# Performance work log

Measured on AMD Instinct MI355X. Metric: run time of the kernel, lower is better.

The kernel has to match this reference:

```python
import jax, jax.numpy as jnp
import numpy as np

LN_EPS = 1e-5


def setup_inputs() -> dict:
    key = jax.random.key(0)
    ks = jax.random.split(key, 6)
    B, M, N, D = 16, 128, 128, 128
    NM, H = 16, 512
    xav = float(np.sqrt(2.0 / (D + D)))  # xavier_normal over (in_dim, out_dim) fan
    return {
        "x": jax.random.normal(ks[0], (B, M, N, D), jnp.float32),
        "w1": jax.random.normal(ks[1], (D, D, NM, 2), jnp.float32) * xav,
        "w2": jax.random.normal(ks[2], (D, D, NM, 2), jnp.float32) * xav,
        "ff_w0": jax.random.normal(ks[3], (D, H), jnp.float32) * float(1.0 / np.sqrt(D)),
        "ff_b0": jnp.zeros((H,), jnp.float32),
        "ff_w1": jax.random.normal(ks[4], (H, D), jnp.float32) * float(1.0 / np.sqrt(H)),
        "ff_b1": jnp.zeros((D,), jnp.float32),
        "ln_g": jnp.ones((D,), jnp.float32),
        "ln_b": jnp.zeros((D,), jnp.float32),
    }


def _layer_norm(h, g, b):
    mu = jnp.mean(h, axis=-1, keepdims=True)
    var = jnp.mean(jnp.square(h - mu), axis=-1, keepdims=True)
    return (h - mu) * jax.lax.rsqrt(var + LN_EPS) * g + b


def _forward_fourier(x, w1, w2):
    # x: [B, M, N, I] -> [B, I, M, N]
    xt = jnp.transpose(x, (0, 3, 1, 2))
    B, I, M, N = xt.shape
    nm = w1.shape[2]
    cw1 = w1[..., 0] + 1j * w1[..., 1]  # [I, O, nm]
    cw2 = w2[..., 0] + 1j * w2[..., 1]
    O = cw1.shape[1]

    # Fourier along last axis (y)
    fty = jnp.fft.rfft(xt, axis=-1, norm="ortho")                    # [B,I,M,N//2+1]
    f1 = jnp.einsum("bixy,ioy->boxy", fty[..., :nm], cw1)            # [B,O,M,nm]
    pad_y = jnp.zeros((B, O, M, N // 2 + 1 - nm), dtype=f1.dtype)
    xy = jnp.fft.irfft(jnp.concatenate([f1, pad_y], axis=-1), n=N, axis=-1, norm="ortho")

    # Fourier along second-to-last axis (x)
    ftx = jnp.fft.rfft(xt, axis=-2, norm="ortho")                    # [B,I,M//2+1,N]
    f2 = jnp.einsum("bixy,iox->boxy", ftx[:, :, :nm, :], cw2)        # [B,O,nm,N]
    pad_x = jnp.zeros((B, O, M // 2 + 1 - nm, N), dtype=f2.dtype)
    xx = jnp.fft.irfft(jnp.concatenate([f2, pad_x], axis=-2), n=M, axis=-2, norm="ortho")

    return jnp.transpose(xx + xy, (0, 2, 3, 1))  # [B,M,N,O]


def reference(x, w1, w2, ff_w0, ff_b0, ff_w1, ff_b1, ln_g, ln_b):
    h = _forward_fourier(x, w1, w2)
    # backcast FeedForward: Linear -> ReLU -> Linear -> LayerNorm (dropout=0)
    h1 = jax.nn.relu(jnp.einsum("bmni,ih->bmnh", h, ff_w0) + ff_b0)
    h2 = jnp.einsum("bmnh,ho->bmno", h1, ff_w1) + ff_b1
    return _layer_norm(h2, ln_g, ln_b)
```

## Files before the change

kernel.cpp:

```cpp
#include <hip/hip_runtime.h>


#define LN_EPS 1e-5f
#define NMODES 16
#define FROW 4096
#define HROW 16384

typedef __attribute__((ext_vector_type(8))) short short8;
typedef __attribute__((ext_vector_type(4))) float f32x4;

__device__ __forceinline__ ushort f2bf(float f) {
    unsigned u = __float_as_uint(f);
    unsigned r = (u + 0x7FFFu + ((u >> 16) & 1u)) >> 16;
    return (ushort)r;
}

__global__ void k_setup(float* __restrict__ Tc, float* __restrict__ Ts,
                        float* __restrict__ IT) {
    const float invs = 0.08838834764831845f;
    for (int idx = threadIdx.x; idx < NMODES * 128; idx += blockDim.x) {
        int k = idx >> 7, n = idx & 127;
        int p = (k * n) & 127;
        float th = (float)p * (6.283185307179586f / 128.0f);
        float c = cosf(th), s = sinf(th);
        Tc[idx] = c * invs;
        Ts[idx] = -s * invs;
        float ck = (k == 0) ? invs : 2.0f * invs;
        IT[n * 32 + 2 * k]     = ck * c;
        IT[n * 32 + 2 * k + 1] = -ck * s;
    }
}

__global__ void k_wpack(const float* __restrict__ w, float* __restrict__ Wp) {
    int idx = blockIdx.x * 256 + threadIdx.x;
    int k  = idx >> 16;
    int ip = (idx >> 8) & 255;
    int op = idx & 255;
    int i = ip & 127, o = op & 127;
    const float* base = w + (((i << 7) | o) * NMODES + k) * 2;
    float re = base[0], im = base[1];
    float v = (ip < 128) ? ((op < 128) ? re : im)
                         : ((op < 128) ? -im : re);
    Wp[idx] = v;
}

__global__ __launch_bounds__(256) void k_wcvt(const float* __restrict__ w0,
        const float* __restrict__ w1, ushort* __restrict__ w0t,
        ushort* __restrict__ w1t) {
    int idx = blockIdx.x * 256 + threadIdx.x;
    int h = idx >> 7, k = idx & 127;
    w0t[idx] = f2bf(w0[k * 512 + h]);
    int o = idx >> 9, hh = idx & 511;
    w1t[idx] = f2bf(w1[hh * 128 + o]);
}

__global__ __launch_bounds__(128) void k_fft(const float* __restrict__ x,
        const float* __restrict__ Tc, const float* __restrict__ Ts,
        float* __restrict__ F, int mode) {
    __shared__ float Tc_s[NMODES * 128];
    __shared__ float Ts_s[NMODES * 128];
    for (int e = threadIdx.x; e < NMODES * 128; e += 128) {
        Tc_s[e] = Tc[e];
        Ts_s[e] = Ts[e];
    }
    __syncthreads();
    int row = blockIdx.x;
    int base, ts;
    if (mode == 0) { base = row * HROW; ts = 128; }
    else { base = (row >> 7) * 2097152 + (row & 127) * 128; ts = 16384; }
    int i = threadIdx.x;
    float re[NMODES], im[NMODES];
#pragma unroll
    for (int k = 0; k < NMODES; ++k) { re[k] = 0.f; im[k] = 0.f; }
    for (int tb = 0; tb < 32; ++tb) {
        int t0 = tb * 4;
        float xv0 = x[base + (t0 + 0) * ts + i];
        float xv1 = x[base + (t0 + 1) * ts + i];
        float xv2 = x[base + (t0 + 2) * ts + i];
        float xv3 = x[base + (t0 + 3) * ts + i];
#pragma unroll
        for (int k = 0; k < NMODES; ++k) {
            f32x4 c4 = *(const f32x4*)&Tc_s[k * 128 + t0];
            f32x4 s4 = *(const f32x4*)&Ts_s[k * 128 + t0];
            re[k] += xv0 * c4[0] + xv1 * c4[1] + xv2 * c4[2] + xv3 * c4[3];
            im[k] += xv0 * s4[0] + xv1 * s4[1] + xv2 * s4[2] + xv3 * s4[3];
        }
    }
    float* outp = F + row * FROW;
#pragma unroll
    for (int k = 0; k < NMODES; ++k) {
        outp[k * 256 + i]       = re[k];
        outp[k * 256 + 128 + i] = im[k];
    }
}

__global__ __launch_bounds__(256) void k_mix(const float* __restrict__ A,
        const float* __restrict__ Wp, float* __restrict__ outF) {
    __shared__ float A_s[256 * 36];
    int kt = blockIdx.x & 15;
    int bm0 = (blockIdx.x >> 4) * 32;
    for (int e = threadIdx.x; e < 32 * 256; e += 256) {
        int r = e >> 8, c = e & 255;
        A_s[c * 36 + r] = A[(bm0 + r) * FROW + kt * 256 + c];
    }
    __syncthreads();
    int tc = threadIdx.x & 63, tr = threadIdx.x >> 6;
    float acc[8][4];
#pragma unroll
    for (int j = 0; j < 8; ++j)
#pragma unroll
        for (int q = 0; q < 4; ++q) acc[j][q] = 0.f;
    const float* wp = Wp + kt * 65536 + tc * 4;
    for (int kk = 0; kk < 256; ++kk) {
        f32x4 wv = *(const f32x4*)(wp + kk * 256);
        f32x4 a0 = *(const f32x4*)&A_s[kk * 36 + tr * 8];
        f32x4 a1 = *(const f32x4*)&A_s[kk * 36 + tr * 8 + 4];
#pragma unroll
        for (int q = 0; q < 4; ++q) {
            acc[0][q] += a0[0] * wv[q]; acc[1][q] += a0[1] * wv[q];
            acc[2][q] += a0[2] * wv[q]; acc[3][q] += a0[3] * wv[q];
            acc[4][q] += a1[0] * wv[q]; acc[5][q] += a1[1] * wv[q];
            acc[6][q] += a1[2] * wv[q]; acc[7][q] += a1[3] * wv[q];
        }
    }
#pragma unroll
    for (int j = 0; j < 8; ++j) {
        f32x4 v = { acc[j][0], acc[j][1], acc[j][2], acc[j][3] };
        *(f32x4*)&outF[(bm0 + tr * 8 + j) * FROW + kt * 256 + tc * 4] = v;
    }
}

__global__ __launch_bounds__(256) void k_icdft(const float* __restrict__ f,
        const float* __restrict__ IT, float* __restrict__ h, int mode) {
    __shared__ float IT_s[128 * 32];
    __shared__ float f_s[32 * 128];
    int row = blockIdx.x;
    for (int e = threadIdx.x; e < 4096; e += 256) {
        IT_s[e] = IT[e];
        f_s[e]  = f[row * FROW + e];
    }
    __syncthreads();
    int o = threadIdx.x & 127, nh = threadIdx.x >> 7;
    int outbase, ostride;
    if (mode == 0) { outbase = row * HROW + o; ostride = 128; }
    else { outbase = (row >> 7) * 2097152 + (row & 127) * 128 + o; ostride = 16384; }
    for (int nb = 0; nb < 8; ++nb) {
        int n0 = nh * 64 + nb * 8;
        float acc[8];
#pragma unroll
        for (int j = 0; j < 8; ++j) acc[j] = 0.f;
#pragma unroll
        for (int kpb = 0; kpb < 8; ++kpb) {
            int kp0 = kpb * 4;
            float f0 = f_s[kp0 * 128 + o];
            float f1v = f_s[kp0 * 128 + 128 + o];
            float f2v = f_s[kp0 * 128 + 256 + o];
            float f3v = f_s[kp0 * 128 + 384 + o];
#pragma unroll
            for (int j = 0; j < 8; ++j) {
                f32x4 it = *(const f32x4*)&IT_s[(n0 + j) * 32 + kp0];
                acc[j] += f0 * it[0] + f1v * it[1] + f2v * it[2] + f3v * it[3];
            }
        }
        if (mode == 0) {
#pragma unroll
            for (int j = 0; j < 8; ++j) h[outbase + (n0 + j) * ostride] = acc[j];
        } else {
#pragma unroll
            for (int j = 0; j < 8; ++j) h[outbase + (n0 + j) * ostride] += acc[j];
        }
    }
}

__global__ __launch_bounds__(256) void k_ffn(float* __restrict__ hio,
        const ushort* __restrict__ w0t, const float* __restrict__ b0,
        const ushort* __restrict__ w1t, const float* __restrict__ b1,
        const float* __restrict__ g, const float* __restrict__ bb) {
    __shared__ __align__(16) char smem[33792 + 1024 + 512];
    ushort* h1_s = (ushort*)smem;
    float*  h2_s = (float*)smem;
    float*  gb_s = (float*)(smem + 33792);
    float*  mr_s = (float*)(smem + 34816);

    int tid = threadIdx.x;
    int R0 = blockIdx.x * 64;
    if (tid < 128) { gb_s[tid] = g[tid]; gb_s[128 + tid] = bb[tid]; }

    int lane = tid & 63, wid = tid >> 6;
    int frow = lane & 15;
    int fk8 = (lane >> 4) * 8;
    int fr4 = (lane >> 4) * 4;

    short8 a1f[4][4];
#pragma unroll
    for (int tr = 0; tr < 4; ++tr)
#pragma unroll
        for (int kk = 0; kk < 4; ++kk) {
            const float* src = &hio[(R0 + tr * 16 + frow) * 128 + kk * 32 + fk8];
            f32x4 v0 = *(const f32x4*)src;
            f32x4 v1 = *(const f32x4*)(src + 4);
            short8 t;
#pragma unroll
            for (int j = 0; j < 4; ++j) {
                t[j]     = (short)f2bf(v0[j]);
                t[4 + j] = (short)f2bf(v1[j]);
            }
            a1f[tr][kk] = t;
        }

    f32x4 acc2[4][2];
#pragma unroll
    for (int a = 0; a < 4; ++a)
#pragma unroll
        for (int c = 0; c < 2; ++c) acc2[a][c] = {0.f, 0.f, 0.f, 0.f};

    for (int hc = 0; hc < 2; ++hc) {
        __syncthreads();
#pragma unroll
        for (int tc = 0; tc < 4; ++tc) {
            int hcol = hc * 256 + wid * 64 + tc * 16 + frow;
            short8 bfr[4];
#pragma unroll
            for (int kk = 0; kk < 4; ++kk)
                bfr[kk] = *(const short8*)&w0t[hcol * 128 + kk * 32 + fk8];
            f32x4 acc1[4];
#pragma unroll
            for (int a = 0; a < 4; ++a) acc1[a] = {0.f, 0.f, 0.f, 0.f};
#pragma unroll
            for (int kk = 0; kk < 4; ++kk)
#pragma unroll
                for (int tr = 0; tr < 4; ++tr)
                    acc1[tr] = __builtin_amdgcn_mfma_f32_16x16x32_bf16(
                        a1f[tr][kk], bfr[kk], acc1[tr], 0, 0, 0);
            float b0v = b0[hcol];
            int lcol = wid * 64 + tc * 16 + frow;
#pragma unroll
            for (int tr = 0; tr < 4; ++tr)
#pragma unroll
                for (int r = 0; r < 4; ++r) {
                    float v = acc1[tr][r] + b0v;
                    h1_s[(tr * 16 + fr4 + r) * 264 + lcol] = f2bf(fmaxf(v, 0.f));
                }
        }
        __syncthreads();
#pragma unroll
        for (int kk = 0; kk < 8; ++kk) {
            short8 a2[4];
#pragma unroll
            for (int tr = 0; tr < 4; ++tr)
                a2[tr] = *(const short8*)&h1_s[(tr * 16 + frow) * 264 + kk * 32 + fk8];
#pragma unroll
            for (int tc = 0; tc < 2; ++tc) {
                int ocol = wid * 32 + tc * 16 + frow;
                short8 b2 = *(const short8*)&w1t[ocol * 512 + hc * 256 + kk * 32 + fk8];
#pragma unroll
                for (int tr = 0; tr < 4; ++tr)
                    acc2[tr][tc] = __builtin_amdgcn_mfma_f32_16x16x32_bf16(
                        a2[tr], b2, acc2[tr][tc], 0, 0, 0);
            }
        }
    }
    __syncthreads();
#pragma unroll
    for (int tc = 0; tc < 2; ++tc) {
        int ocol = wid * 32 + tc * 16 + frow;
        float b1v = b1[ocol];
#pragma unroll
        for (int tr = 0; tr < 4; ++tr)
#pragma unroll
            for (int r = 0; r < 4; ++r)
                h2_s[(tr * 16 + fr4 + r) * 132 + ocol] = acc2[tr][tc][r] + b1v;
    }
    __syncthreads();
    int row = tid >> 2, sub = tid & 3;
    const float* hr = &h2_s[row * 132 + sub * 32];
    float s = 0.f;
#pragma unroll
    for (int j = 0; j < 32; ++j) s += hr[j];
    s += __shfl_xor(s, 1); s += __shfl_xor(s, 2);
    float mu = s * (1.0f / 128.0f);
    float s2 = 0.f;
#pragma unroll
    for (int j = 0; j < 32; ++j) { float dv = hr[j] - mu; s2 += dv * dv; }
    s2 += __shfl_xor(s2, 1); s2 += __shfl_xor(s2, 2);
    float rstd = rsqrtf(s2 * (1.0f / 128.0f) + LN_EPS);
    if (sub == 0) { mr_s[row * 2] = mu; mr_s[row * 2 + 1] = rstd; }
    __syncthreads();
    for (int e = tid; e < 2048; e += 256) {
        int r = e >> 5, d4 = (e & 31) * 4;
        float mu2 = mr_s[r * 2], rs = mr_s[r * 2 + 1];
        f32x4 v = *(const f32x4*)&h2_s[r * 132 + d4];
        f32x4 o;
#pragma unroll
        for (int j = 0; j < 4; ++j)
            o[j] = (v[j] - mu2) * rs * gb_s[d4 + j] + gb_s[128 + d4 + j];
        *(f32x4*)&hio[(R0 + r) * 128 + d4] = o;
    }
}

extern "C" void kernel_launch(void* const* d_in, const int* in_sizes, int n_in,
                              void* d_out, int out_size, void* d_ws, size_t ws_size,
                              hipStream_t stream) {
    (void)in_sizes; (void)n_in; (void)out_size; (void)ws_size;
    const float* x   = (const float*)d_in[0];
    const float* w1  = (const float*)d_in[1];
    const float* w2  = (const float*)d_in[2];
    const float* fw0 = (const float*)d_in[3];
    const float* fb0 = (const float*)d_in[4];
    const float* fw1 = (const float*)d_in[5];
    const float* fb1 = (const float*)d_in[6];
    const float* lng = (const float*)d_in[7];
    const float* lnb = (const float*)d_in[8];
    float* out = (float*)d_out;

    char* ws = (char*)d_ws;
    float* Tc   = (float*)(ws);
    float* Ts   = (float*)(ws + 8192);
    float* IT   = (float*)(ws + 16384);
    float* Wp   = (float*)(ws + 32768);
    float* buf0 = (float*)(ws + 32768 + 4194304);
    float* buf1 = (float*)(ws + 32768 + 4194304 + 33554432);

    k_setup<<<1, 256, 0, stream>>>(Tc, Ts, IT);

    k_wpack<<<4096, 256, 0, stream>>>(w1, Wp);
    k_fft  <<<2048, 128, 0, stream>>>(x, Tc, Ts, buf0, 0);
    k_mix  <<<1024, 256, 0, stream>>>(buf0, Wp, buf1);
    k_icdft<<<2048, 256, 0, stream>>>(buf1, IT, out, 0);

    k_wpack<<<4096, 256, 0, stream>>>(w2, Wp);
    k_fft  <<<2048, 128, 0, stream>>>(x, Tc, Ts, buf0, 1);
    k_mix  <<<1024, 256, 0, stream>>>(buf0, Wp, buf1);

    ushort* w0t = (ushort*)buf0;
    ushort* w1t = (ushort*)(buf0 + 65536);
    k_wcvt <<<256, 256, 0, stream>>>(fw0, fw1, w0t, w1t);

    k_icdft<<<2048, 256, 0, stream>>>(buf1, IT, out, 1);

    k_ffn<<<4096, 256, 0, stream>>>(out, w0t, fb0, w1t, fb1, lng, lnb);
}
```

Measured before the change: 585.2 us.

## Move spectral mixing onto bf16x3 MFMA and fuse LayerNorm into FFN registers

The fp32 FMA spectral mixing GEMM is replaced by an MFMA version that splits operands into bf16 hi/lo pairs and uses three products to keep near-fp32 accuracy. Weights are packed transposed into hi/lo bf16 buffers. The FFN kernel now processes the hidden dimension in four chunks with a smaller shared-memory tile, caches biases in LDS, and computes LayerNorm statistics directly from accumulators via shuffles using a one-pass sum/sum-of-squares, avoiding the h2 staging round trip. Risks include slight precision loss from the split-bf16 scheme and the single-pass variance formula.

```diff
diff --git a/kernel.cpp b/kernel.cpp
--- a/kernel.cpp
+++ b/kernel.cpp
@@ -7,12 +7,16 @@
 #define HROW 16384
 
 typedef __attribute__((ext_vector_type(8))) short short8;
+typedef __attribute__((ext_vector_type(4))) short short4v;
 typedef __attribute__((ext_vector_type(4))) float f32x4;
 
 __device__ __forceinline__ ushort f2bf(float f) {
     unsigned u = __float_as_uint(f);
     unsigned r = (u + 0x7FFFu + ((u >> 16) & 1u)) >> 16;
     return (ushort)r;
+}
+__device__ __forceinline__ float bf2f(ushort h) {
+    return __uint_as_float(((unsigned)h) << 16);
 }
 
 __global__ void k_setup(float* __restrict__ Tc, float* __restrict__ Ts,
@@ -31,17 +35,21 @@
     }
 }
 
-__global__ void k_wpack(const float* __restrict__ w, float* __restrict__ Wp) {
+__global__ void k_wpack(const float* __restrict__ w, ushort* __restrict__ Wph,
+                        ushort* __restrict__ Wpl) {
     int idx = blockIdx.x * 256 + threadIdx.x;
     int k  = idx >> 16;
-    int ip = (idx >> 8) & 255;
-    int op = idx & 255;
+    int op = (idx >> 8) & 255;
+    int ip = idx & 255;
     int i = ip & 127, o = op & 127;
     const float* base = w + (((i << 7) | o) * NMODES + k) * 2;
     float re = base[0], im = base[1];
     float v = (ip < 128) ? ((op < 128) ? re : im)
                          : ((op < 128) ? -im : re);
-    Wp[idx] = v;
+    ushort hi = f2bf(v);
+    ushort lo = f2bf(v - bf2f(hi));
+    Wph[idx] = hi;
+    Wpl[idx] = lo;
 }
 
 __global__ __launch_bounds__(256) void k_wcvt(const float* __restrict__ w0,
@@ -94,40 +102,71 @@
     }
 }
 
-__global__ __launch_bounds__(256) void k_mix(const float* __restrict__ A,
-        const float* __restrict__ Wp, float* __restrict__ outF) {
-    __shared__ float A_s[256 * 36];
+__global__ __launch_bounds__(256) void k_mixm(const float* __restrict__ A,
+        const ushort* __restrict__ Wph, const ushort* __restrict__ Wpl,
+        float* __restrict__ outF) {
+    __shared__ ushort Ah[32 * 264];
+    __shared__ ushort Al[32 * 264];
+    int tid = threadIdx.x;
     int kt = blockIdx.x & 15;
     int bm0 = (blockIdx.x >> 4) * 32;
-    for (int e = threadIdx.x; e < 32 * 256; e += 256) {
-        int r = e >> 8, c = e & 255;
-        A_s[c * 36 + r] = A[(bm0 + r) * FROW + kt * 256 + c];
-    }
-    __syncthreads();
-    int tc = threadIdx.x & 63, tr = threadIdx.x >> 6;
-    float acc[8][4];
-#pragma unroll
-    for (int j = 0; j < 8; ++j)
-#pragma unroll
-        for (int q = 0; q < 4; ++q) acc[j][q] = 0.f;
-    const float* wp = Wp + kt * 65536 + tc * 4;
-    for (int kk = 0; kk < 256; ++kk) {
-        f32x4 wv = *(const f32x4*)(wp + kk * 256);
-        f32x4 a0 = *(const f32x4*)&A_s[kk * 36 + tr * 8];
-        f32x4 a1 = *(const f32x4*)&A_s[kk * 36 + tr * 8 + 4];
-#pragma unroll
-        for (int q = 0; q < 4; ++q) {
-            acc[0][q] += a0[0] * wv[q]; acc[1][q] += a0[1] * wv[q];
-            acc[2][q] += a0[2] * wv[q]; acc[3][q] += a0[3] * wv[q];
-            acc[4][q] += a1[0] * wv[q]; acc[5][q] += a1[1] * wv[q];
-            acc[6][q] += a1[2] * wv[q]; acc[7][q] += a1[3] * wv[q];
-        }
-    }
-#pragma unroll
-    for (int j = 0; j < 8; ++j) {
-        f32x4 v = { acc[j][0], acc[j][1], acc[j][2], acc[j][3] };
-        *(f32x4*)&outF[(bm0 + tr * 8 + j) * FROW + kt * 256 + tc * 4] = v;
-    }
+    {
+        int row = tid >> 3, cg = tid & 7;
+        const float* arow = A + (bm0 + row) * FROW + kt * 256 + cg * 32;
+        ushort* ah = &Ah[row * 264 + cg * 32];
+        ushort* al = &Al[row * 264 + cg * 32];
+#pragma unroll
+        for (int j = 0; j < 8; ++j) {
+            f32x4 v = *(const f32x4*)(arow + j * 4);
+            short4v h4, l4;
+#pragma unroll
+            for (int q = 0; q < 4; ++q) {
+                ushort h = f2bf(v[q]);
+                h4[q] = (short)h;
+                l4[q] = (short)f2bf(v[q] - bf2f(h));
+            }
+            *(short4v*)(ah + j * 4) = h4;
+            *(short4v*)(al + j * 4) = l4;
+        }
+    }
+    __syncthreads();
+    int lane = tid & 63, wid = tid >> 6;
+    int frow = lane & 15, fk8 = (lane >> 4) * 8, fr4 = (lane >> 4) * 4;
+    f32x4 acc[2][4];
+#pragma unroll
+    for (int a = 0; a < 2; ++a)
+#pragma unroll
+        for (int c = 0; c < 4; ++c) acc[a][c] = {0.f, 0.f, 0.f, 0.f};
+    const ushort* wph = Wph + kt * 65536;
+    const ushort* wpl = Wpl + kt * 65536;
+#pragma unroll
+    for (int kk = 0; kk < 8; ++kk) {
+        short8 ah0 = *(const short8*)&Ah[(frow)      * 264 + kk * 32 + fk8];
+        short8 ah1 = *(const short8*)&Ah[(16 + frow) * 264 + kk * 32 + fk8];
+        short8 al0 = *(const short8*)&Al[(frow)      * 264 + kk * 32 + fk8];
+        short8 al1 = *(const short8*)&Al[(16 + frow) * 264 + kk * 32 + fk8];
+#pragma unroll
+        for (int tc = 0; tc < 4; ++tc) {
+            int op = wid * 64 + tc * 16 + frow;
+            int base = op * 256 + kk * 32 + fk8;
+            short8 wh = *(const short8*)&wph[base];
+            short8 wl = *(const short8*)&wpl[base];
+            acc[0][tc] = __builtin_amdgcn_mfma_f32_16x16x32_bf16(ah0, wh, acc[0][tc], 0, 0, 0);
+            acc[0][tc] = __builtin_amdgcn_mfma_f32_16x16x32_bf16(ah0, wl, acc[0][tc], 0, 0, 0);
+            acc[0][tc] = __builtin_amdgcn_mfma_f32_16x16x32_bf16(al0, wh, acc[0][tc], 0, 0, 0);
+            acc[1][tc] = __builtin_amdgcn_mfma_f32_16x16x32_bf16(ah1, wh, acc[1][tc], 0, 0, 0);
+            acc[1][tc] = __builtin_amdgcn_mfma_f32_16x16x32_bf16(ah1, wl, acc[1][tc], 0, 0, 0);
+            acc[1][tc] = __builtin_amdgcn_mfma_f32_16x16x32_bf16(al1, wh, acc[1][tc], 0, 0, 0);
+        }
+    }
+#pragma unroll
+    for (int tr = 0; tr < 2; ++tr)
+#pragma unroll
+        for (int tc = 0; tc < 4; ++tc)
+#pragma unroll
+            for (int r = 0; r < 4; ++r)
+                outF[(bm0 + tr * 16 + fr4 + r) * FROW + kt * 256 + wid * 64 + tc * 16 + frow]
+                    = acc[tr][tc][r];
 }
 
 __global__ __launch_bounds__(256) void k_icdft(const float* __restrict__ f,
@@ -176,15 +215,22 @@
         const ushort* __restrict__ w0t, const float* __restrict__ b0,
         const ushort* __restrict__ w1t, const float* __restrict__ b1,
         const float* __restrict__ g, const float* __restrict__ bb) {
-    __shared__ __align__(16) char smem[33792 + 1024 + 512];
-    ushort* h1_s = (ushort*)smem;
-    float*  h2_s = (float*)smem;
-    float*  gb_s = (float*)(smem + 33792);
-    float*  mr_s = (float*)(smem + 34816);
+    __shared__ __align__(16) ushort h1_s[64 * 136];
+    __shared__ float b0_s[512];
+    __shared__ float gb_s[256];
+    __shared__ float b1_s[128];
+    __shared__ float ps_s[64 * 4];
+    __shared__ float pq_s[64 * 4];
+    __shared__ float mr_s[64 * 2];
 
     int tid = threadIdx.x;
     int R0 = blockIdx.x * 64;
-    if (tid < 128) { gb_s[tid] = g[tid]; gb_s[128 + tid] = bb[tid]; }
+    for (int e = tid; e < 512; e += 256) b0_s[e] = b0[e];
+    if (tid < 128) {
+        gb_s[tid] = g[tid];
+        gb_s[128 + tid] = bb[tid];
+        b1_s[tid] = b1[tid];
+    }
 
     int lane = tid & 63, wid = tid >> 6;
     int frow = lane & 15;
@@ -214,11 +260,12 @@
 #pragma unroll
         for (int c = 0; c < 2; ++c) acc2[a][c] = {0.f, 0.f, 0.f, 0.f};
 
-    for (int hc = 0; hc < 2; ++hc) {
+    for (int hc = 0; hc < 4; ++hc) {
         __syncthreads();
 #pragma unroll
-        for (int tc = 0; tc < 4; ++tc) {
-            int hcol = hc * 256 + wid * 64 + tc * 16 + frow;
+        for (int tc = 0; tc < 2; ++tc) {
+            int lcol = wid * 32 + tc * 16 + frow;
+            int hcol = hc * 128 + lcol;
             short8 bfr[4];
 #pragma unroll
             for (int kk = 0; kk < 4; ++kk)
@@ -232,27 +279,26 @@
                 for (int tr = 0; tr < 4; ++tr)
                     acc1[tr] = __builtin_amdgcn_mfma_f32_16x16x32_bf16(
                         a1f[tr][kk], bfr[kk], acc1[tr], 0, 0, 0);
-            float b0v = b0[hcol];
-            int lcol = wid * 64 + tc * 16 + frow;
+            float b0v = b0_s[hcol];
 #pragma unroll
             for (int tr = 0; tr < 4; ++tr)
 #pragma unroll
                 for (int r = 0; r < 4; ++r) {
                     float v = acc1[tr][r] + b0v;
-                    h1_s[(tr * 16 + fr4 + r) * 264 + lcol] = f2bf(fmaxf(v, 0.f));
+                    h1_s[(tr * 16 + fr4 + r) * 136 + lcol] = f2bf(fmaxf(v, 0.f));
                 }
         }
         __syncthreads();
 #pragma unroll
-        for (int kk = 0; kk < 8; ++kk) {
+        for (int kk = 0; kk < 4; ++kk) {
             short8 a2[4];
 #pragma unroll
             for (int tr = 0; tr < 4; ++tr)
-                a2[tr] = *(const short8*)&h1_s[(tr * 16 + frow) * 264 + kk * 32 + fk8];
+                a2[tr] = *(const short8*)&h1_s[(tr * 16 + frow) * 136 + kk * 32 + fk8];
 #pragma unroll
             for (int tc = 0; tc < 2; ++tc) {
                 int ocol = wid * 32 + tc * 16 + frow;
-                short8 b2 = *(const short8*)&w1t[ocol * 512 + hc * 256 + kk * 32 + fk8];
+                short8 b2 = *(const short8*)&w1t[ocol * 512 + hc * 128 + kk * 32 + fk8];
 #pragma unroll
                 for (int tr = 0; tr < 4; ++tr)
                     acc2[tr][tc] = __builtin_amdgcn_mfma_f32_16x16x32_bf16(
@@ -260,42 +306,50 @@
             }
         }
     }
-    __syncthreads();
-#pragma unroll
-    for (int tc = 0; tc < 2; ++tc) {
-        int ocol = wid * 32 + tc * 16 + frow;
-        float b1v = b1[ocol];
-#pragma unroll
-        for (int tr = 0; tr < 4; ++tr)
-#pragma unroll
-            for (int r = 0; r < 4; ++r)
-                h2_s[(tr * 16 + fr4 + r) * 132 + ocol] = acc2[tr][tc][r] + b1v;
-    }
-    __syncthreads();
-    int row = tid >> 2, sub = tid & 3;
-    const float* hr = &h2_s[row * 132 + sub * 32];
-    float s = 0.f;
-#pragma unroll
-    for (int j = 0; j < 32; ++j) s += hr[j];
-    s += __shfl_xor(s, 1); s += __shfl_xor(s, 2);
-    float mu = s * (1.0f / 128.0f);
-    float s2 = 0.f;
-#pragma unroll
-    for (int j = 0; j < 32; ++j) { float dv = hr[j] - mu; s2 += dv * dv; }
-    s2 += __shfl_xor(s2, 1); s2 += __shfl_xor(s2, 2);
-    float rstd = rsqrtf(s2 * (1.0f / 128.0f) + LN_EPS);
-    if (sub == 0) { mr_s[row * 2] = mu; mr_s[row * 2 + 1] = rstd; }
-    __syncthreads();
-    for (int e = tid; e < 2048; e += 256) {
-        int r = e >> 5, d4 = (e & 31) * 4;
-        float mu2 = mr_s[r * 2], rs = mr_s[r * 2 + 1];
-        f32x4 v = *(const f32x4*)&h2_s[r * 132 + d4];
-        f32x4 o;
-#pragma unroll
-        for (int j = 0; j < 4; ++j)
-            o[j] = (v[j] - mu2) * rs * gb_s[d4 + j] + gb_s[128 + d4 + j];
-        *(f32x4*)&hio[(R0 + r) * 128 + d4] = o;
-    }
+    float b1v0 = b1_s[wid * 32 + frow];
+    float b1v1 = b1_s[wid * 32 + 16 + frow];
+#pragma unroll
+    for (int tr = 0; tr < 4; ++tr)
+#pragma unroll
+        for (int r = 0; r < 4; ++r) {
+            float v0 = acc2[tr][0][r] + b1v0;
+            float v1 = acc2[tr][1][r] + b1v1;
+            acc2[tr][0][r] = v0;
+            acc2[tr][1][r] = v1;
+            float s = v0 + v1;
+            float q = v0 * v0 + v1 * v1;
+            s += __shfl_xor(s, 1); q += __shfl_xor(q, 1);
+            s += __shfl_xor(s, 2); q += __shfl_xor(q, 2);
+            s += __shfl_xor(s, 4); q += __shfl_xor(q, 4);
+            s += __shfl_xor(s, 8); q += __shfl_xor(q, 8);
+            if (frow == 0) {
+                int row_l = tr * 16 + fr4 + r;
+                ps_s[row_l * 4 + wid] = s;
+                pq_s[row_l * 4 + wid] = q;
+            }
+        }
+    __syncthreads();
+    if (tid < 64) {
+        float S = ps_s[tid * 4] + ps_s[tid * 4 + 1] + ps_s[tid * 4 + 2] + ps_s[tid * 4 + 3];
+        float Q = pq_s[tid * 4] + pq_s[tid * 4 + 1] + pq_s[tid * 4 + 2] + pq_s[tid * 4 + 3];
+        float mu = S * (1.0f / 128.0f);
+        float var = Q * (1.0f / 128.0f) - mu * mu;
+        mr_s[tid * 2] = mu;
+        mr_s[tid * 2 + 1] = rsqrtf(fmaxf(var, 0.f) + LN_EPS);
+    }
+    __syncthreads();
+    float g0 = gb_s[wid * 32 + frow],       bb0 = gb_s[128 + wid * 32 + frow];
+    float g1 = gb_s[wid * 32 + 16 + frow],  bb1 = gb_s[128 + wid * 32 + 16 + frow];
+#pragma unroll
+    for (int tr = 0; tr < 4; ++tr)
+#pragma unroll
+        for (int r = 0; r < 4; ++r) {
+            int row_l = tr * 16 + fr4 + r;
+            float mu = mr_s[row_l * 2], rs = mr_s[row_l * 2 + 1];
+            float* orow = &hio[(R0 + row_l) * 128 + wid * 32];
+            orow[frow]      = (acc2[tr][0][r] - mu) * rs * g0 + bb0;
+            orow[16 + frow] = (acc2[tr][1][r] - mu) * rs * g1 + bb1;
+        }
 }
 
 extern "C" void kernel_launch(void* const* d_in, const int* in_sizes, int n_in,
@@ -314,28 +368,27 @@
     float* out = (float*)d_out;
 
     char* ws = (char*)d_ws;
-    float* Tc   = (float*)(ws);
-    float* Ts   = (float*)(ws + 8192);
-    float* IT   = (float*)(ws + 16384);
-    float* Wp   = (float*)(ws + 32768);
-    float* buf0 = (float*)(ws + 32768 + 4194304);
-    float* buf1 = (float*)(ws + 32768 + 4194304 + 33554432);
+    float*  Tc  = (float*)(ws);
+    float*  Ts  = (float*)(ws + 8192);
+    float*  IT  = (float*)(ws + 16384);
+    ushort* Wph = (ushort*)(ws + 32768);
+    ushort* Wpl = (ushort*)(ws + 32768 + 2097152);
+    ushort* w0t = (ushort*)(ws + 4227072);
+    ushort* w1t = (ushort*)(ws + 4358144);
+    float*  buf0 = (float*)(ws + 4489216);
+    float*  buf1 = (float*)(ws + 4489216 + 33554432);
 
     k_setup<<<1, 256, 0, stream>>>(Tc, Ts, IT);
-
-    k_wpack<<<4096, 256, 0, stream>>>(w1, Wp);
+    k_wcvt <<<256, 256, 0, stream>>>(fw0, fw1, w0t, w1t);
+
+    k_wpack<<<4096, 256, 0, stream>>>(w1, Wph, Wpl);
     k_fft  <<<2048, 128, 0, stream>>>(x, Tc, Ts, buf0, 0);
-    k_mix  <<<1024, 256, 0, stream>>>(buf0, Wp, buf1);
+    k_mixm <<<1024, 256, 0, stream>>>(buf0, Wph, Wpl, buf1);
     k_icdft<<<2048, 256, 0, stream>>>(buf1, IT, out, 0);
 
-    k_wpack<<<4096, 256, 0, stream>>>(w2, Wp);
+    k_wpack<<<4096, 256, 0, stream>>>(w2, Wph, Wpl);
     k_fft  <<<2048, 128, 0, stream>>>(x, Tc, Ts, buf0, 1);
-    k_mix  <<<1024, 256, 0, stream>>>(buf0, Wp, buf1);
-
-    ushort* w0t = (ushort*)buf0;
-    ushort* w1t = (ushort*)(buf0 + 65536);
-    k_wcvt <<<256, 256, 0, stream>>>(fw0, fw1, w0t, w1t);
-
+    k_mixm <<<1024, 256, 0, stream>>>(buf0, Wph, Wpl, buf1);
     k_icdft<<<2048, 256, 0, stream>>>(buf1, IT, out, 1);
 
     k_ffn<<<4096, 256, 0, stream>>>(out, w0t, fb0, w1t, fb1, lng, lnb);
```

Result: faster. 564.0 us (-3.6%).
